# Optimization experiments

Hardware: AMD Instinct MI355X
Metric: run time of the kernel (lower is better)

Reference implementation:

```python
import jax, jax.numpy as jnp
import numpy as np

N_NODES = 50000
N_EDGES = 640000
IN_SIZE = 512
HID1 = 128


def setup_inputs() -> dict:
    key = jax.random.key(0)
    ks = jax.random.split(key, 7)
    x = jax.random.normal(ks[0], (N_NODES, IN_SIZE), dtype=jnp.float32)
    edge_index = jax.random.randint(ks[1], (2, N_EDGES), 0, N_NODES, dtype=jnp.int64)
    # Linear params stored as (in, out) so y = x @ W + b (equiv to torch x @ W.T + b)
    s_enc = 1.0 / np.sqrt(IN_SIZE)
    s_dec = 1.0 / np.sqrt(HID1)
    W_enc = jax.random.uniform(ks[2], (IN_SIZE, HID1), jnp.float32, -s_enc, s_enc)
    b_enc = jax.random.uniform(ks[3], (HID1,), jnp.float32, -s_enc, s_enc)
    W_dec = jax.random.uniform(ks[4], (HID1, IN_SIZE), jnp.float32, -s_dec, s_dec)
    b_dec = jax.random.uniform(ks[5], (IN_SIZE,), jnp.float32, -s_dec, s_dec)
    gcn_bias = jnp.zeros((HID1,), dtype=jnp.float32)  # reset_parameters zeroes it
    return {"x": x, "W_enc": W_enc, "b_enc": b_enc, "W_dec": W_dec,
            "b_dec": b_dec, "gcn_bias": gcn_bias, "edge_index": edge_index}


def gcn_conv(h, edge_index, bias):
    # GCNConv with lin.weight frozen to identity (in==out), so lin is a no-op.
    N = h.shape[0]
    loops = jnp.arange(N, dtype=edge_index.dtype)
    row = jnp.concatenate([edge_index[0], loops])  # source nodes (x_j)
    col = jnp.concatenate([edge_index[1], loops])  # target nodes (aggregation)
    deg = jax.ops.segment_sum(jnp.ones_like(col, dtype=h.dtype), col, num_segments=N)
    dinv = jnp.where(deg > 0, jax.lax.rsqrt(deg), jnp.zeros_like(deg))
    norm = dinv[row] * dinv[col]              # [E+N]
    msg = norm[:, None] * h[row]              # gather + scale, [E+N, HID1]
    out = jax.ops.segment_sum(msg, col, num_segments=N)  # scatter-add
    return out + bias


def reference(x, W_enc, b_enc, W_dec, b_dec, gcn_bias, edge_index):
    encoded = jax.nn.relu(x @ W_enc + b_enc)          # [N, HID1]
    messaged = gcn_conv(encoded, edge_index, gcn_bias)
    decoded = jax.nn.sigmoid(messaged @ W_dec + b_dec)  # [N, IN_SIZE]
    return decoded
```

## Files before the change

### kernel.cpp

```cpp
#include <hip/hip_runtime.h>
#include <math.h>

#define NNODES 50000
#define NEDGES 640000
#define INSZ 512
#define HID 128
#define NBLK ((NNODES + 255) / 256)

typedef short s16x8 __attribute__((ext_vector_type(8)));
typedef float f32x4 __attribute__((ext_vector_type(4)));

static __device__ inline short f2bf(float f) {
    __bf16 b = (__bf16)f;
    return __builtin_bit_cast(short, b);
}
static __device__ inline float bf2f(unsigned short u) {
    unsigned int i = (unsigned int)u << 16;
    return __builtin_bit_cast(float, i);
}

__global__ __launch_bounds__(256) void prep_weights(const float* __restrict__ We,
                                                    const float* __restrict__ Wd,
                                                    short* __restrict__ WTe,
                                                    short* __restrict__ WTd) {
    int t = blockIdx.x * 256 + threadIdx.x;
    if (t < INSZ * HID) {
        int n = t & (HID - 1);
        int k = t >> 7;
        WTe[n * INSZ + k] = f2bf(We[t]);
    } else {
        int u = t - INSZ * HID;
        int n = u & (INSZ - 1);
        int k = u >> 9;
        WTd[n * HID + k] = f2bf(Wd[u]);
    }
}

__global__ __launch_bounds__(256) void count_kernel(const int* __restrict__ col,
                                                    int* __restrict__ counts) {
    int e = blockIdx.x * blockDim.x + threadIdx.x;
    if (e < NEDGES) atomicAdd(&counts[col[e]], 1);
}

__global__ __launch_bounds__(256) void partial_kernel(const int* __restrict__ counts,
                                                      int* __restrict__ blocksums) {
    int i = blockIdx.x * 256 + threadIdx.x;
    int v = (i < NNODES) ? counts[i] : 0;
#pragma unroll
    for (int off = 32; off; off >>= 1) v += __shfl_down(v, off, 64);
    __shared__ int ws[4];
    if ((threadIdx.x & 63) == 0) ws[threadIdx.x >> 6] = v;
    __syncthreads();
    if (threadIdx.x == 0) blocksums[blockIdx.x] = ws[0] + ws[1] + ws[2] + ws[3];
}

__global__ __launch_bounds__(256) void scan_blocks(const int* __restrict__ blocksums,
                                                   int* __restrict__ blockoffs) {
    __shared__ int s[256];
    const int t = threadIdx.x;
    s[t] = (t < NBLK) ? blocksums[t] : 0;
    __syncthreads();
    for (int off = 1; off < 256; off <<= 1) {
        int u = (t >= off) ? s[t - off] : 0;
        __syncthreads();
        s[t] += u;
        __syncthreads();
    }
    blockoffs[t] = (t == 0) ? 0 : s[t - 1];
}

__global__ __launch_bounds__(256) void scan_final(const int* __restrict__ counts,
                                                  const int* __restrict__ blockoffs,
                                                  int* __restrict__ starts,
                                                  int* __restrict__ cursor,
                                                  float* __restrict__ dinv) {
    __shared__ int s[256];
    const int t = threadIdx.x;
    const int i = blockIdx.x * 256 + t;
    int v = (i < NNODES) ? counts[i] : 0;
    s[t] = v;
    __syncthreads();
    for (int off = 1; off < 256; off <<= 1) {
        int u = (t >= off) ? s[t - off] : 0;
        __syncthreads();
        s[t] += u;
        __syncthreads();
    }
    int excl = ((t == 0) ? 0 : s[t - 1]) + blockoffs[blockIdx.x];
    if (i < NNODES) {
        starts[i] = excl;
        cursor[i] = excl;
        dinv[i] = rsqrtf((float)v + 1.0f);
        if (i == NNODES - 1) starts[NNODES] = excl + v;
    }
}

__global__ __launch_bounds__(256) void scatter_kernel(const int* __restrict__ erow,
                                                      const int* __restrict__ ecol,
                                                      int* __restrict__ cursor,
                                                      int* __restrict__ csr_row) {
    int e = blockIdx.x * blockDim.x + threadIdx.x;
    if (e < NEDGES) {
        int pos = atomicAdd(&cursor[ecol[e]], 1);
        csr_row[pos] = erow[e];
    }
}

#define XPAD 72
__global__ __launch_bounds__(256) void encoder_mfma(const float* __restrict__ x,
                                                    const short* __restrict__ WT,
                                                    const float* __restrict__ b,
                                                    unsigned short* __restrict__ h) {
    __shared__ short xs[2][64 * XPAD];
    const int t    = threadIdx.x;
    const int lane = t & 63;
    const int wv   = t >> 6;
    const int r16  = lane & 15;
    const int kg   = lane >> 4;
    const int mbase = blockIdx.x * 64;
    const int nb    = wv * 32;

    const float4* sp[4];
    int sdst[4];
#pragma unroll
    for (int j = 0; j < 4; ++j) {
        int c = j * 256 + t;
        int row = c >> 4, c4 = c & 15;
        int gr = mbase + row; if (gr >= NNODES) gr = NNODES - 1;
        sp[j]   = (const float4*)x + (size_t)gr * (INSZ / 4) + c4;
        sdst[j] = row * XPAD + c4 * 4;
    }

    f32x4 acc[4][2] = {};
    float4 rB[4], rC[4];

    {
        float4 rA[4];
#pragma unroll
        for (int j = 0; j < 4; ++j) rA[j] = sp[j][0];
#pragma unroll
        for (int j = 0; j < 4; ++j) {
            short4 w;
            w.x = f2bf(rA[j].x); w.y = f2bf(rA[j].y);
            w.z = f2bf(rA[j].z); w.w = f2bf(rA[j].w);
            *(short4*)&xs[0][sdst[j]] = w;
        }
    }
    __syncthreads();
#pragma unroll
    for (int j = 0; j < 4; ++j) rB[j] = sp[j][16];

#pragma unroll 2
    for (int ks = 0; ks < 8; ++ks) {
        const int cur = ks & 1;
        if (ks < 6) {
#pragma unroll
            for (int j = 0; j < 4; ++j) rC[j] = sp[j][(ks + 2) * 16];
        }
#pragma unroll
        for (int kk = 0; kk < 2; ++kk) {
            s16x8 a[4], bb[2];
#pragma unroll
            for (int mt = 0; mt < 4; ++mt)
                a[mt] = *(const s16x8*)&xs[cur][(mt * 16 + r16) * XPAD + kk * 32 + kg * 8];
#pragma unroll
            for (int nt = 0; nt < 2; ++nt)
                bb[nt] = *(const s16x8*)(WT + (size_t)(nb + nt * 16 + r16) * INSZ + ks * 64 + kk * 32 + kg * 8);
#pragma unroll
            for (int mt = 0; mt < 4; ++mt)
#pragma unroll
                for (int nt = 0; nt < 2; ++nt)
                    acc[mt][nt] = __builtin_amdgcn_mfma_f32_16x16x32_bf16(a[mt], bb[nt], acc[mt][nt], 0, 0, 0);
        }
        if (ks < 7) {
#pragma unroll
            for (int j = 0; j < 4; ++j) {
                short4 w;
                w.x = f2bf(rB[j].x); w.y = f2bf(rB[j].y);
                w.z = f2bf(rB[j].z); w.w = f2bf(rB[j].w);
                *(short4*)&xs[cur ^ 1][sdst[j]] = w;
            }
#pragma unroll
            for (int j = 0; j < 4; ++j) rB[j] = rC[j];
        }
        __syncthreads();
    }

    const int ro = kg * 4;
#pragma unroll
    for (int mt = 0; mt < 4; ++mt) {
        const int row0 = mbase + mt * 16 + ro;
#pragma unroll
        for (int nt = 0; nt < 2; ++nt) {
            const int col = nb + nt * 16 + r16;
            const float bj = b[col];
#pragma unroll
            for (int v = 0; v < 4; ++v) {
                int rr = row0 + v;
                if (rr < NNODES)
                    h[(size_t)rr * HID + col] = (unsigned short)f2bf(fmaxf(acc[mt][nt][v] + bj, 0.0f));
            }
        }
    }
}

__global__ __launch_bounds__(256) void aggregate_csr_kernel(const int* __restrict__ starts,
                                                            const int* __restrict__ csr_row,
                                                            const float* __restrict__ dinv,
                                                            const unsigned short* __restrict__ h,
                                                            unsigned short* __restrict__ agg) {
    const int node = (blockIdx.x * 256 + threadIdx.x) >> 5;
    const int l32  = threadIdx.x & 31;
    if (node >= NNODES) return;
    const float dc = dinv[node];
    const int s0 = starts[node], s1 = starts[node + 1];
    const ushort4* hp = (const ushort4*)h;

    ushort4 sv = hp[(size_t)node * 32 + l32];
    const float sc = dc * dc;
    float4 acc;
    acc.x = bf2f(sv.x) * sc; acc.y = bf2f(sv.y) * sc;
    acc.z = bf2f(sv.z) * sc; acc.w = bf2f(sv.w) * sc;

    int i = s0;
    for (; i + 7 < s1; i += 8) {
        int r[8]; float nn[8]; ushort4 hv[8];
#pragma unroll
        for (int j = 0; j < 8; ++j) r[j] = csr_row[i + j];
#pragma unroll
        for (int j = 0; j < 8; ++j) hv[j] = hp[(size_t)r[j] * 32 + l32];
#pragma unroll
        for (int j = 0; j < 8; ++j) nn[j] = dinv[r[j]] * dc;
#pragma unroll
        for (int j = 0; j < 8; ++j) {
            acc.x = fmaf(nn[j], bf2f(hv[j].x), acc.x);
            acc.y = fmaf(nn[j], bf2f(hv[j].y), acc.y);
            acc.z = fmaf(nn[j], bf2f(hv[j].z), acc.z);
            acc.w = fmaf(nn[j], bf2f(hv[j].w), acc.w);
        }
    }
    for (; i + 3 < s1; i += 4) {
        int r[4]; float nn[4]; ushort4 hv[4];
#pragma unroll
        for (int j = 0; j < 4; ++j) r[j] = csr_row[i + j];
#pragma unroll
        for (int j = 0; j < 4; ++j) hv[j] = hp[(size_t)r[j] * 32 + l32];
#pragma unroll
        for (int j = 0; j < 4; ++j) nn[j] = dinv[r[j]] * dc;
#pragma unroll
        for (int j = 0; j < 4; ++j) {
            acc.x = fmaf(nn[j], bf2f(hv[j].x), acc.x);
            acc.y = fmaf(nn[j], bf2f(hv[j].y), acc.y);
            acc.z = fmaf(nn[j], bf2f(hv[j].z), acc.z);
            acc.w = fmaf(nn[j], bf2f(hv[j].w), acc.w);
        }
    }
    for (; i < s1; ++i) {
        int r = csr_row[i];
        float nrm = dinv[r] * dc;
        ushort4 hv = hp[(size_t)r * 32 + l32];
        acc.x = fmaf(nrm, bf2f(hv.x), acc.x); acc.y = fmaf(nrm, bf2f(hv.y), acc.y);
        acc.z = fmaf(nrm, bf2f(hv.z), acc.z); acc.w = fmaf(nrm, bf2f(hv.w), acc.w);
    }
    ushort4 ov;
    ov.x = (unsigned short)f2bf(acc.x); ov.y = (unsigned short)f2bf(acc.y);
    ov.z = (unsigned short)f2bf(acc.z); ov.w = (unsigned short)f2bf(acc.w);
    ((ushort4*)agg)[(size_t)node * 32 + l32] = ov;
}

#define APAD 136
#define EP2  36
__global__ __launch_bounds__(512) void decoder_mfma(const unsigned short* __restrict__ agg,
                                                    const float* __restrict__ gb,
                                                    const short* __restrict__ WT,
                                                    const float* __restrict__ b,
                                                    float* __restrict__ out) {
    __shared__ short as_lds[64 * APAD];
    __shared__ float ep[8][16 * EP2];
    const int t    = threadIdx.x;
    const int lane = t & 63;
    const int wv   = t >> 6;
    const int r16  = lane & 15;
    const int kg   = lane >> 4;
    const int l8   = lane & 7;
    const int lr8  = lane >> 3;
    const int mbase = blockIdx.x * 64;
    const int nwb   = wv * 64;

    {
        const int row = t >> 3;
        const int f0  = (t & 7) * 16;
        int gr = mbase + row; if (gr >= NNODES) gr = NNODES - 1;
        const ushort4* src4 = (const ushort4*)(agg + (size_t)gr * HID + f0);
        const float4*  g4   = (const float4*)(gb + f0);
        short4* d4 = (short4*)(as_lds + row * APAD + f0);
#pragma unroll
        for (int j = 0; j < 4; ++j) {
            ushort4 u = src4[j];
            float4 g = g4[j];
            short4 w;
            w.x = f2bf(bf2f(u.x) + g.x); w.y = f2bf(bf2f(u.y) + g.y);
            w.z = f2bf(bf2f(u.z) + g.z); w.w = f2bf(bf2f(u.w) + g.w);
            d4[j] = w;
        }
    }
    __syncthreads();

    f32x4 acc[4][4] = {};
#pragma unroll
    for (int ks = 0; ks < 4; ++ks) {
        s16x8 a[4], bb[4];
#pragma unroll
        for (int mt = 0; mt < 4; ++mt)
            a[mt] = *(const s16x8*)&as_lds[(mt * 16 + r16) * APAD + ks * 32 + kg * 8];
#pragma unroll
        for (int nt = 0; nt < 4; ++nt)
            bb[nt] = *(const s16x8*)(WT + (size_t)(nwb + nt * 16 + r16) * HID + ks * 32 + kg * 8);
#pragma unroll
        for (int mt = 0; mt < 4; ++mt)
#pragma unroll
            for (int nt = 0; nt < 4; ++nt)
                acc[mt][nt] = __builtin_amdgcn_mfma_f32_16x16x32_bf16(a[mt], bb[nt], acc[mt][nt], 0, 0, 0);
    }

    float bj[4];
#pragma unroll
    for (int nt = 0; nt < 4; ++nt) bj[nt] = b[nwb + nt * 16 + r16];

    float* eps = ep[wv];
#pragma unroll
    for (int mt = 0; mt < 4; ++mt) {
#pragma unroll
        for (int half = 0; half < 2; ++half) {
#pragma unroll
            for (int ntl = 0; ntl < 2; ++ntl) {
                const int nt = half * 2 + ntl;
#pragma unroll
                for (int v = 0; v < 4; ++v) {
                    float z = acc[mt][nt][v] + bj[nt];
                    eps[(kg * 4 + v) * EP2 + ntl * 16 + r16] = 1.0f / (1.0f + __expf(-z));
                }
            }
#pragma unroll
            for (int p = 0; p < 2; ++p) {
                const int row = p * 8 + lr8;
                float4 vv = *(const float4*)&eps[row * EP2 + l8 * 4];
                const int rr = mbase + mt * 16 + row;
                if (rr < NNODES)
                    *(float4*)&out[(size_t)rr * INSZ + nwb + half * 32 + l8 * 4] = vv;
            }
        }
    }
}

extern "C" void kernel_launch(void* const* d_in, const int* in_sizes, int n_in,
                              void* d_out, int out_size, void* d_ws, size_t ws_size,
                              hipStream_t stream) {
    const float* x        = (const float*)d_in[0];
    const float* W_enc    = (const float*)d_in[1];
    const float* b_enc    = (const float*)d_in[2];
    const float* W_dec    = (const float*)d_in[3];
    const float* b_dec    = (const float*)d_in[4];
    const float* gcn_bias = (const float*)d_in[5];
    const int*   edge     = (const int*)d_in[6];
    const int*   erow = edge;
    const int*   ecol = edge + NEDGES;

    float* out = (float*)d_out;
    unsigned short* agg = (unsigned short*)d_ws;
    float* dinv  = (float*)(agg + (size_t)NNODES * HID);
    short* wdecT = (short*)(dinv + NNODES);
    unsigned short* h = (unsigned short*)out;
    int*   csr_row   = (int*)(out + (size_t)NNODES * HID);
    int*   starts    = csr_row + NEDGES;
    int*   counts    = starts + NNODES + 1;
    int*   cursor    = counts + NNODES;
    int*   blocksums = cursor + NNODES;
    int*   blockoffs = blocksums + 256;
    short* wencT     = (short*)(blockoffs + 256);

    hipMemsetAsync(counts, 0, (size_t)NNODES * sizeof(int), stream);
    prep_weights<<<(2 * INSZ * HID + 255) / 256, 256, 0, stream>>>(W_enc, W_dec, wencT, wdecT);
    count_kernel<<<(NEDGES + 255) / 256, 256, 0, stream>>>(ecol, counts);
    partial_kernel<<<NBLK, 256, 0, stream>>>(counts, blocksums);
    scan_blocks<<<1, 256, 0, stream>>>(blocksums, blockoffs);
    scan_final<<<NBLK, 256, 0, stream>>>(counts, blockoffs, starts, cursor, dinv);
    scatter_kernel<<<(NEDGES + 255) / 256, 256, 0, stream>>>(erow, ecol, cursor, csr_row);
    encoder_mfma<<<(NNODES + 63) / 64, 256, 0, stream>>>(x, wencT, b_enc, h);
    aggregate_csr_kernel<<<((size_t)NNODES * 32 + 255) / 256, 256, 0, stream>>>(starts, csr_row, dinv, h, agg);
    decoder_mfma<<<(NNODES + 63) / 64, 512, 0, stream>>>(agg, gcn_bias, wdecT, b_dec, out);
}
```

Baseline: 187.5 us.

## Stream encoder x tiles directly into LDS with global_load_lds and swizzle

The encoder GEMM now loads fp32 x tiles straight from global memory into LDS using the async global_load_lds builtin, replacing the register-staged prefetch plus bf16 convert-and-store. LDS holds fp32 with an XOR swizzle on 16-byte chunks to avoid bank conflicts, and the bf16 conversion moves to the point where MFMA operands are read. The row tile per block shrinks from 64 to 32, doubling the grid. This is meant to cut register pressure and staging instructions and to raise occupancy, at the cost of twice the LDS bytes per row, more reloads of W per output row, and redundant conversion work.

After: 190.4 us. Within noise of the previous version (+1.5%).

```diff
diff --git a/kernel.cpp b/kernel.cpp
--- a/kernel.cpp
+++ b/kernel.cpp
@@ -17,6 +17,11 @@
 static __device__ inline float bf2f(unsigned short u) {
     unsigned int i = (unsigned int)u << 16;
     return __builtin_bit_cast(float, i);
+}
+static __device__ inline void gload16(const float* g, float* l) {
+    __builtin_amdgcn_global_load_lds(
+        (const __attribute__((address_space(1))) void*)g,
+        (__attribute__((address_space(3))) void*)l, 16, 0, 0);
 }
 
 __global__ __launch_bounds__(256) void prep_weights(const float* __restrict__ We,
@@ -106,89 +111,77 @@
     }
 }
 
-#define XPAD 72
 __global__ __launch_bounds__(256) void encoder_mfma(const float* __restrict__ x,
                                                     const short* __restrict__ WT,
                                                     const float* __restrict__ b,
                                                     unsigned short* __restrict__ h) {
-    __shared__ short xs[2][64 * XPAD];
+    __shared__ float xs[2][32 * 64];
     const int t    = threadIdx.x;
     const int lane = t & 63;
     const int wv   = t >> 6;
     const int r16  = lane & 15;
     const int kg   = lane >> 4;
-    const int mbase = blockIdx.x * 64;
+    const int mbase = blockIdx.x * 32;
     const int nb    = wv * 32;
 
-    const float4* sp[4];
-    int sdst[4];
-#pragma unroll
-    for (int j = 0; j < 4; ++j) {
-        int c = j * 256 + t;
-        int row = c >> 4, c4 = c & 15;
-        int gr = mbase + row; if (gr >= NNODES) gr = NNODES - 1;
-        sp[j]   = (const float4*)x + (size_t)gr * (INSZ / 4) + c4;
-        sdst[j] = row * XPAD + c4 * 4;
-    }
-
-    f32x4 acc[4][2] = {};
-    float4 rB[4], rC[4];
-
-    {
-        float4 rA[4];
-#pragma unroll
-        for (int j = 0; j < 4; ++j) rA[j] = sp[j][0];
-#pragma unroll
-        for (int j = 0; j < 4; ++j) {
-            short4 w;
-            w.x = f2bf(rA[j].x); w.y = f2bf(rA[j].y);
-            w.z = f2bf(rA[j].z); w.w = f2bf(rA[j].w);
-            *(short4*)&xs[0][sdst[j]] = w;
-        }
-    }
-    __syncthreads();
-#pragma unroll
-    for (int j = 0; j < 4; ++j) rB[j] = sp[j][16];
-
-#pragma unroll 2
+    const float* gsrc[2];
+    float* ldstA[2];
+    float* ldstB[2];
+#pragma unroll
+    for (int i = 0; i < 2; ++i) {
+        const int rbase = wv * 8 + i * 4;
+        int gr = mbase + rbase + (lane >> 4);
+        if (gr >= NNODES) gr = NNODES - 1;
+        const int sch = (lane & 15) ^ (gr & 7);
+        gsrc[i]  = x + (size_t)gr * INSZ + sch * 4;
+        ldstA[i] = &xs[0][rbase * 64];
+        ldstB[i] = &xs[1][rbase * 64];
+    }
+
+#pragma unroll
+    for (int i = 0; i < 2; ++i) gload16(gsrc[i], ldstA[i]);
+    __syncthreads();
+
+    f32x4 acc[2][2] = {};
+#pragma unroll
     for (int ks = 0; ks < 8; ++ks) {
         const int cur = ks & 1;
-        if (ks < 6) {
-#pragma unroll
-            for (int j = 0; j < 4; ++j) rC[j] = sp[j][(ks + 2) * 16];
-        }
+        if (ks < 7) {
+#pragma unroll
+            for (int i = 0; i < 2; ++i)
+                gload16(gsrc[i] + (ks + 1) * 64, cur ? ldstA[i] : ldstB[i]);
+        }
+        const float* xb = xs[cur];
 #pragma unroll
         for (int kk = 0; kk < 2; ++kk) {
-            s16x8 a[4], bb[2];
-#pragma unroll
-            for (int mt = 0; mt < 4; ++mt)
-                a[mt] = *(const s16x8*)&xs[cur][(mt * 16 + r16) * XPAD + kk * 32 + kg * 8];
+            s16x8 a[2], bb[2];
+#pragma unroll
+            for (int mt = 0; mt < 2; ++mt) {
+                const int r  = mt * 16 + r16;
+                const int g0 = kk * 8 + kg * 2;
+                const float* base = xb + r * 64;
+                f32x4 f0 = *(const f32x4*)(base + ((g0       ^ (r & 7)) * 4));
+                f32x4 f1 = *(const f32x4*)(base + (((g0 + 1) ^ (r & 7)) * 4));
+                s16x8 w;
+                w[0] = f2bf(f0[0]); w[1] = f2bf(f0[1]); w[2] = f2bf(f0[2]); w[3] = f2bf(f0[3]);
+                w[4] = f2bf(f1[0]); w[5] = f2bf(f1[1]); w[6] = f2bf(f1[2]); w[7] = f2bf(f1[3]);
+                a[mt] = w;
+            }
 #pragma unroll
             for (int nt = 0; nt < 2; ++nt)
                 bb[nt] = *(const s16x8*)(WT + (size_t)(nb + nt * 16 + r16) * INSZ + ks * 64 + kk * 32 + kg * 8);
 #pragma unroll
-            for (int mt = 0; mt < 4; ++mt)
+            for (int mt = 0; mt < 2; ++mt)
 #pragma unroll
                 for (int nt = 0; nt < 2; ++nt)
                     acc[mt][nt] = __builtin_amdgcn_mfma_f32_16x16x32_bf16(a[mt], bb[nt], acc[mt][nt], 0, 0, 0);
         }
-        if (ks < 7) {
-#pragma unroll
-            for (int j = 0; j < 4; ++j) {
-                short4 w;
-                w.x = f2bf(rB[j].x); w.y = f2bf(rB[j].y);
-                w.z = f2bf(rB[j].z); w.w = f2bf(rB[j].w);
-                *(short4*)&xs[cur ^ 1][sdst[j]] = w;
-            }
-#pragma unroll
-            for (int j = 0; j < 4; ++j) rB[j] = rC[j];
-        }
         __syncthreads();
     }
 
     const int ro = kg * 4;
 #pragma unroll
-    for (int mt = 0; mt < 4; ++mt) {
+    for (int mt = 0; mt < 2; ++mt) {
         const int row0 = mbase + mt * 16 + ro;
 #pragma unroll
         for (int nt = 0; nt < 2; ++nt) {
@@ -386,7 +379,7 @@
     scan_blocks<<<1, 256, 0, stream>>>(blocksums, blockoffs);
     scan_final<<<NBLK, 256, 0, stream>>>(counts, blockoffs, starts, cursor, dinv);
     scatter_kernel<<<(NEDGES + 255) / 256, 256, 0, stream>>>(erow, ecol, cursor, csr_row);
-    encoder_mfma<<<(NNODES + 63) / 64, 256, 0, stream>>>(x, wencT, b_enc, h);
+    encoder_mfma<<<(NNODES + 31) / 32, 256, 0, stream>>>(x, wencT, b_enc, h);
     aggregate_csr_kernel<<<((size_t)NNODES * 32 + 255) / 256, 256, 0, stream>>>(starts, csr_row, dinv, h, agg);
     decoder_mfma<<<(NNODES + 63) / 64, 512, 0, stream>>>(agg, gcn_bias, wdecT, b_dec, out);
 }
```
